# Performance work log

Measured on AMD Instinct MI355X. Metric: run time of the kernel, lower is better.

The kernel has to match this reference:

```python
import math
import jax, jax.numpy as jnp
import numpy as np

B, Q, K, D = 32, 1024, 1024, 128
MASK_VALUE = -1000000.0


def setup_inputs() -> dict:
    key = jax.random.key(0)
    kq, kk, kv, kl = jax.random.split(key, 4)
    return {
        "queries": jax.random.normal(kq, (B, Q, D), dtype=jnp.float32),
        "keys": jax.random.normal(kk, (B, K, D), dtype=jnp.float32),
        "values": jax.random.normal(kv, (B, K, D), dtype=jnp.float32),
        "valid_lens": jax.random.randint(kl, (B,), 1, K + 1, dtype=jnp.int32),
    }


def reference(queries, keys, values, valid_lens):
    d = queries.shape[-1]
    # scores: [B, Q, K]
    scores = jnp.einsum("bqd,bkd->bqk", queries, keys) / math.sqrt(d)
    # key-padding mask: position k valid iff k < valid_lens[b] (broadcast over queries)
    mask = jnp.arange(keys.shape[1])[None, None, :] < valid_lens[:, None, None]
    scores = jnp.where(mask, scores, MASK_VALUE)
    attn = jax.nn.softmax(scores, axis=-1)
    # dropout p=0.0 -> identity
    return jnp.einsum("bqk,bkv->bqv", attn, values)
```

## Files before the change

kernel.cpp:

```cpp
#include <hip/hip_runtime.h>
#include <math.h>

typedef _Float16 f16;
typedef __attribute__((ext_vector_type(8))) _Float16 f16x8;
typedef __attribute__((ext_vector_type(4))) _Float16 f16x4;
typedef __attribute__((ext_vector_type(4))) float f32x4;

constexpr int BATCH = 32;
constexpr int QL = 1024;
constexpr int KL = 1024;
constexpr int D = 128;
constexpr int BQ = 64;
constexpr int BK = 64;
constexpr int DKP = 136;
constexpr int BKP = 72;

#define CSC 0.12752863187087177f

__global__ __launch_bounds__(256, 3)
void attn_fwd(const float* __restrict__ Qp, const float* __restrict__ Kp,
              const float* __restrict__ Vp, const int* __restrict__ VLp,
              float* __restrict__ Op) {
  __shared__ f16 sK[BK][DKP];
  __shared__ f16 sVT[D][BKP];
  __shared__ f16 sP[4][16][BKP];

  const int tid  = threadIdx.x;
  const int wave = tid >> 6, lane = tid & 63;
  const int l16  = lane & 15, quad = lane >> 4;
  const int b = blockIdx.y, qt = blockIdx.x;
  const int vl = VLp[b];

  const float* Qb = Qp + ((size_t)(b * QL + qt * BQ + wave * 16 + l16)) * D;
  f16x8 qfrag[4];
  #pragma unroll
  for (int kc = 0; kc < 4; ++kc) {
    const float* p = Qb + kc * 32 + quad * 8;
    float4 u = *(const float4*)p;
    float4 v = *(const float4*)(p + 4);
    f16x8 f;
    f[0] = (f16)u.x; f[1] = (f16)u.y; f[2] = (f16)u.z; f[3] = (f16)u.w;
    f[4] = (f16)v.x; f[5] = (f16)v.y; f[6] = (f16)v.z; f[7] = (f16)v.w;
    qfrag[kc] = f;
  }

  float m2[4] = {-INFINITY, -INFINITY, -INFINITY, -INFINITY};
  float lsum[4] = {0.f, 0.f, 0.f, 0.f};
  f32x4 o[8];
  #pragma unroll
  for (int dt = 0; dt < 8; ++dt) o[dt] = (f32x4){0.f, 0.f, 0.f, 0.f};

  const float* Kb = Kp + (size_t)b * KL * D;
  const float* Vb = Vp + (size_t)b * KL * D;
  const int ntiles = (vl + BK - 1) / BK;

  for (int t = 0; t < ntiles; ++t) {
    __syncthreads();

    {
      const float4* Kt = (const float4*)(Kb + (size_t)t * BK * D);
      #pragma unroll
      for (int i = 0; i < 8; ++i) {
        int f = tid + i * 256;
        int row = f >> 5, c4 = f & 31;
        float4 u = Kt[f];
        f16x4 h;
        h[0] = (f16)u.x; h[1] = (f16)u.y; h[2] = (f16)u.z; h[3] = (f16)u.w;
        *(f16x4*)&sK[row][c4 * 4] = h;
      }
      const float* Vt = Vb + (size_t)t * BK * D;
      #pragma unroll
      for (int i = 0; i < 2; ++i) {
        int f = tid + i * 256;
        int rq = f & 15;
        int c4 = f >> 4;
        const float* base = Vt + (size_t)(rq * 4) * D + c4 * 4;
        float4 r0 = *(const float4*)(base);
        float4 r1 = *(const float4*)(base + D);
        float4 r2 = *(const float4*)(base + 2 * D);
        float4 r3 = *(const float4*)(base + 3 * D);
        int d0 = c4 * 4, k0 = rq * 4;
        f16x4 h;
        h[0] = (f16)r0.x; h[1] = (f16)r1.x; h[2] = (f16)r2.x; h[3] = (f16)r3.x;
        *(f16x4*)&sVT[d0 + 0][k0] = h;
        h[0] = (f16)r0.y; h[1] = (f16)r1.y; h[2] = (f16)r2.y; h[3] = (f16)r3.y;
        *(f16x4*)&sVT[d0 + 1][k0] = h;
        h[0] = (f16)r0.z; h[1] = (f16)r1.z; h[2] = (f16)r2.z; h[3] = (f16)r3.z;
        *(f16x4*)&sVT[d0 + 2][k0] = h;
        h[0] = (f16)r0.w; h[1] = (f16)r1.w; h[2] = (f16)r2.w; h[3] = (f16)r3.w;
        *(f16x4*)&sVT[d0 + 3][k0] = h;
      }
    }
    __syncthreads();

    f32x4 s[4];
    #pragma unroll
    for (int ct = 0; ct < 4; ++ct) {
      f32x4 c = (f32x4){0.f, 0.f, 0.f, 0.f};
      #pragma unroll
      for (int kc = 0; kc < 4; ++kc) {
        f16x8 kf = *(const f16x8*)&sK[ct * 16 + l16][kc * 32 + quad * 8];
        c = __builtin_amdgcn_mfma_f32_16x16x32_f16(qfrag[kc], kf, c, 0, 0, 0);
      }
      s[ct] = c;
    }

    #pragma unroll
    for (int ct = 0; ct < 4; ++ct) {
      int kk = t * BK + ct * 16 + l16;
      bool ok = kk < vl;
      #pragma unroll
      for (int r = 0; r < 4; ++r)
        s[ct][r] = ok ? s[ct][r] * CSC : -1.0e9f;
    }

    float mnew[4], alpha[4], ls[4];
    #pragma unroll
    for (int r = 0; r < 4; ++r) {
      float v = fmaxf(fmaxf(s[0][r], s[1][r]), fmaxf(s[2][r], s[3][r]));
      v = fmaxf(v, __shfl_xor(v, 1));
      v = fmaxf(v, __shfl_xor(v, 2));
      v = fmaxf(v, __shfl_xor(v, 4));
      v = fmaxf(v, __shfl_xor(v, 8));
      mnew[r]  = fmaxf(m2[r], v);
      alpha[r] = __builtin_amdgcn_exp2f(m2[r] - mnew[r]);
      m2[r]    = mnew[r];
      ls[r]    = 0.f;
    }
    #pragma unroll
    for (int ct = 0; ct < 4; ++ct)
      #pragma unroll
      for (int r = 0; r < 4; ++r) {
        float p = __builtin_amdgcn_exp2f(s[ct][r] - mnew[r]);
        s[ct][r] = p;
        ls[r] += p;
      }
    #pragma unroll
    for (int r = 0; r < 4; ++r) {
      float v = ls[r];
      v += __shfl_xor(v, 1);
      v += __shfl_xor(v, 2);
      v += __shfl_xor(v, 4);
      v += __shfl_xor(v, 8);
      lsum[r] = lsum[r] * alpha[r] + v;
    }

    #pragma unroll
    for (int ct = 0; ct < 4; ++ct)
      #pragma unroll
      for (int r = 0; r < 4; ++r)
        sP[wave][quad * 4 + r][ct * 16 + l16] = (f16)s[ct][r];
    #pragma unroll
    for (int dt = 0; dt < 8; ++dt)
      #pragma unroll
      for (int r = 0; r < 4; ++r)
        o[dt][r] *= alpha[r];

    asm volatile("s_waitcnt lgkmcnt(0)" ::: "memory");

    #pragma unroll
    for (int ks = 0; ks < 2; ++ks) {
      f16x8 pf = *(const f16x8*)&sP[wave][l16][ks * 32 + quad * 8];
      #pragma unroll
      for (int dt = 0; dt < 8; ++dt) {
        f16x8 vf = *(const f16x8*)&sVT[dt * 16 + l16][ks * 32 + quad * 8];
        o[dt] = __builtin_amdgcn_mfma_f32_16x16x32_f16(pf, vf, o[dt], 0, 0, 0);
      }
    }
  }

  float* Ob = Op + ((size_t)(b * QL + qt * BQ + wave * 16)) * D;
  #pragma unroll
  for (int r = 0; r < 4; ++r) {
    float inv = 1.0f / lsum[r];
    int row = quad * 4 + r;
    #pragma unroll
    for (int dt = 0; dt < 8; ++dt)
      Ob[(size_t)row * D + dt * 16 + l16] = o[dt][r] * inv;
  }
}

extern "C" void kernel_launch(void* const* d_in, const int* in_sizes, int n_in,
                              void* d_out, int out_size, void* d_ws, size_t ws_size,
                              hipStream_t stream) {
  const float* Qp = (const float*)d_in[0];
  const float* Kp = (const float*)d_in[1];
  const float* Vp = (const float*)d_in[2];
  const int*   VL = (const int*)d_in[3];
  float* Op = (float*)d_out;

  dim3 grid(QL / BQ, BATCH);
  attn_fwd<<<grid, dim3(256), 0, stream>>>(Qp, Kp, Vp, VL, Op);
}
```

Measured before the change: 141.3 us.

## Prefetch next K/V tile into registers, permute K rows, remap block order

Global loads of the next K and V tiles are issued into registers right after the shared-memory writes of the current tile, so the memory latency overlaps the QK and PV MFMA work. K rows are permuted in shared memory so each lane's four score columns are contiguous, which lets the P tile be written as one packed f16x4 store per row, and the mask index is adjusted to match. The grid is flattened and remapped so batches are spread by block id, likely to group blocks across XCDs and caches. The register prefetch adds 64 float registers per thread, which may reduce occupancy below the launch-bounds target.

```diff
diff --git a/kernel.cpp b/kernel.cpp
--- a/kernel.cpp
+++ b/kernel.cpp
@@ -28,8 +28,11 @@
   const int tid  = threadIdx.x;
   const int wave = tid >> 6, lane = tid & 63;
   const int l16  = lane & 15, quad = lane >> 4;
-  const int b = blockIdx.y, qt = blockIdx.x;
-  const int vl = VLp[b];
+
+  const int id  = blockIdx.x;
+  const int b   = (( (id >> 3) & 3) << 3) | (id & 7);
+  const int qt  = id >> 5;
+  const int vl  = VLp[b];
 
   const float* Qb = Qp + ((size_t)(b * QL + qt * BQ + wave * 16 + l16)) * D;
   f16x8 qfrag[4];
@@ -44,7 +47,7 @@
     qfrag[kc] = f;
   }
 
-  float m2[4] = {-INFINITY, -INFINITY, -INFINITY, -INFINITY};
+  float m2[4]   = {-INFINITY, -INFINITY, -INFINITY, -INFINITY};
   float lsum[4] = {0.f, 0.f, 0.f, 0.f};
   f32x4 o[8];
   #pragma unroll
@@ -54,44 +57,68 @@
   const float* Vb = Vp + (size_t)b * KL * D;
   const int ntiles = (vl + BK - 1) / BK;
 
+  float4 kreg[8], vreg[8];
+
+  {
+    const float4* Kt = (const float4*)Kb;
+    #pragma unroll
+    for (int i = 0; i < 8; ++i) kreg[i] = Kt[tid + i * 256];
+    #pragma unroll
+    for (int i = 0; i < 2; ++i) {
+      int f = tid + i * 256;
+      const float* base = Vb + (size_t)((f & 15) * 4) * D + (f >> 4) * 4;
+      vreg[i * 4 + 0] = *(const float4*)(base);
+      vreg[i * 4 + 1] = *(const float4*)(base + D);
+      vreg[i * 4 + 2] = *(const float4*)(base + 2 * D);
+      vreg[i * 4 + 3] = *(const float4*)(base + 3 * D);
+    }
+  }
+
   for (int t = 0; t < ntiles; ++t) {
+    #pragma unroll
+    for (int i = 0; i < 8; ++i) {
+      int f = tid + i * 256;
+      int row = f >> 5, c4 = f & 31;
+      int rp = (row & 3) * 16 + (row >> 2);
+      float4 u = kreg[i];
+      f16x4 h;
+      h[0] = (f16)u.x; h[1] = (f16)u.y; h[2] = (f16)u.z; h[3] = (f16)u.w;
+      *(f16x4*)&sK[rp][c4 * 4] = h;
+    }
+    #pragma unroll
+    for (int i = 0; i < 2; ++i) {
+      int f = tid + i * 256;
+      int k0 = (f & 15) * 4, d0 = (f >> 4) * 4;
+      float4 r0 = vreg[i * 4 + 0], r1 = vreg[i * 4 + 1];
+      float4 r2 = vreg[i * 4 + 2], r3 = vreg[i * 4 + 3];
+      f16x4 h;
+      h[0] = (f16)r0.x; h[1] = (f16)r1.x; h[2] = (f16)r2.x; h[3] = (f16)r3.x;
+      *(f16x4*)&sVT[d0 + 0][k0] = h;
+      h[0] = (f16)r0.y; h[1] = (f16)r1.y; h[2] = (f16)r2.y; h[3] = (f16)r3.y;
+      *(f16x4*)&sVT[d0 + 1][k0] = h;
+      h[0] = (f16)r0.z; h[1] = (f16)r1.z; h[2] = (f16)r2.z; h[3] = (f16)r3.z;
+      *(f16x4*)&sVT[d0 + 2][k0] = h;
+      h[0] = (f16)r0.w; h[1] = (f16)r1.w; h[2] = (f16)r2.w; h[3] = (f16)r3.w;
+      *(f16x4*)&sVT[d0 + 3][k0] = h;
+    }
     __syncthreads();
 
     {
-      const float4* Kt = (const float4*)(Kb + (size_t)t * BK * D);
-      #pragma unroll
-      for (int i = 0; i < 8; ++i) {
-        int f = tid + i * 256;
-        int row = f >> 5, c4 = f & 31;
-        float4 u = Kt[f];
-        f16x4 h;
-        h[0] = (f16)u.x; h[1] = (f16)u.y; h[2] = (f16)u.z; h[3] = (f16)u.w;
-        *(f16x4*)&sK[row][c4 * 4] = h;
-      }
-      const float* Vt = Vb + (size_t)t * BK * D;
+      int tn = (t + 1 < ntiles) ? t + 1 : t;
+      const float4* Kt = (const float4*)(Kb + (size_t)tn * BK * D);
+      #pragma unroll
+      for (int i = 0; i < 8; ++i) kreg[i] = Kt[tid + i * 256];
+      const float* Vt = Vb + (size_t)tn * BK * D;
       #pragma unroll
       for (int i = 0; i < 2; ++i) {
         int f = tid + i * 256;
-        int rq = f & 15;
-        int c4 = f >> 4;
-        const float* base = Vt + (size_t)(rq * 4) * D + c4 * 4;
-        float4 r0 = *(const float4*)(base);
-        float4 r1 = *(const float4*)(base + D);
-        float4 r2 = *(const float4*)(base + 2 * D);
-        float4 r3 = *(const float4*)(base + 3 * D);
-        int d0 = c4 * 4, k0 = rq * 4;
-        f16x4 h;
-        h[0] = (f16)r0.x; h[1] = (f16)r1.x; h[2] = (f16)r2.x; h[3] = (f16)r3.x;
-        *(f16x4*)&sVT[d0 + 0][k0] = h;
-        h[0] = (f16)r0.y; h[1] = (f16)r1.y; h[2] = (f16)r2.y; h[3] = (f16)r3.y;
-        *(f16x4*)&sVT[d0 + 1][k0] = h;
-        h[0] = (f16)r0.z; h[1] = (f16)r1.z; h[2] = (f16)r2.z; h[3] = (f16)r3.z;
-        *(f16x4*)&sVT[d0 + 2][k0] = h;
-        h[0] = (f16)r0.w; h[1] = (f16)r1.w; h[2] = (f16)r2.w; h[3] = (f16)r3.w;
-        *(f16x4*)&sVT[d0 + 3][k0] = h;
-      }
-    }
-    __syncthreads();
+        const float* base = Vt + (size_t)((f & 15) * 4) * D + (f >> 4) * 4;
+        vreg[i * 4 + 0] = *(const float4*)(base);
+        vreg[i * 4 + 1] = *(const float4*)(base + D);
+        vreg[i * 4 + 2] = *(const float4*)(base + 2 * D);
+        vreg[i * 4 + 3] = *(const float4*)(base + 3 * D);
+      }
+    }
 
     f32x4 s[4];
     #pragma unroll
@@ -107,8 +134,7 @@
 
     #pragma unroll
     for (int ct = 0; ct < 4; ++ct) {
-      int kk = t * BK + ct * 16 + l16;
-      bool ok = kk < vl;
+      bool ok = (t * BK + l16 * 4 + ct) < vl;
       #pragma unroll
       for (int r = 0; r < 4; ++r)
         s[ct][r] = ok ? s[ct][r] * CSC : -1.0e9f;
@@ -146,10 +172,12 @@
     }
 
     #pragma unroll
-    for (int ct = 0; ct < 4; ++ct)
-      #pragma unroll
-      for (int r = 0; r < 4; ++r)
-        sP[wave][quad * 4 + r][ct * 16 + l16] = (f16)s[ct][r];
+    for (int r = 0; r < 4; ++r) {
+      f16x4 h;
+      h[0] = (f16)s[0][r]; h[1] = (f16)s[1][r];
+      h[2] = (f16)s[2][r]; h[3] = (f16)s[3][r];
+      *(f16x4*)&sP[wave][quad * 4 + r][l16 * 4] = h;
+    }
     #pragma unroll
     for (int dt = 0; dt < 8; ++dt)
       #pragma unroll
@@ -167,6 +195,7 @@
         o[dt] = __builtin_amdgcn_mfma_f32_16x16x32_f16(pf, vf, o[dt], 0, 0, 0);
       }
     }
+    __syncthreads();
   }
 
   float* Ob = Op + ((size_t)(b * QL + qt * BQ + wave * 16)) * D;
@@ -189,6 +218,5 @@
   const int*   VL = (const int*)d_in[3];
   float* Op = (float*)d_out;
 
-  dim3 grid(QL / BQ, BATCH);
-  attn_fwd<<<grid, dim3(256), 0, stream>>>(Qp, Kp, Vp, VL, Op);
+  attn_fwd<<<dim3(QL / BQ * BATCH), dim3(256), 0, stream>>>(Qp, Kp, Vp, VL, Op);
 }
```

Result: slower. 145.4 us (+2.9%).
